# Kernel optimization log

Hardware: AMD Instinct MI355X
Metric: run time of the kernel (lower is better)

Reference implementation:

```python
import jax, jax.numpy as jnp
import numpy as np
import math

B, S, D, NH, HFF, E, K, C, L, V = 8, 256, 1024, 16, 2048, 8, 2, 10, 4, 32000
HD = D // NH
EPS = 1e-5


def _pos_encoding(max_len, d_model):
    pos = jnp.arange(max_len, dtype=jnp.float32)[:, None]
    div = jnp.exp(jnp.arange(0, d_model, 2, dtype=jnp.float32) * (-math.log(10000.0) / d_model))
    pe = jnp.zeros((max_len, d_model), dtype=jnp.float32)
    pe = pe.at[:, 0::2].set(jnp.sin(pos * div))
    pe = pe.at[:, 1::2].set(jnp.cos(pos * div))
    return pe[:, None, :]  # [max_len, 1, D], matching torch buffer layout


def _layernorm(x, g, b):
    mu = jnp.mean(x, axis=-1, keepdims=True)
    var = jnp.mean((x - mu) ** 2, axis=-1, keepdims=True)
    return (x - mu) * jax.lax.rsqrt(var + EPS) * g + b


def setup_inputs() -> dict:
    key = jax.random.key(0)
    ks = jax.random.split(key, 20)
    sc = lambda *shape: 0.02
    inp = {
        "src": jax.random.randint(ks[0], (B, S), 0, V, dtype=jnp.int32),
        "emb": jax.random.normal(ks[1], (V, D), jnp.float32) * 0.02,
        "in_proj_w": jax.random.normal(ks[2], (L, 3 * D, D), jnp.float32) * 0.02,
        "in_proj_b": jnp.zeros((L, 3 * D), jnp.float32),
        "out_w": jax.random.normal(ks[3], (L, D, D), jnp.float32) * 0.02,
        "out_b": jnp.zeros((L, D), jnp.float32),
        "ln1_g": jnp.ones((L, D), jnp.float32),
        "ln1_b": jnp.zeros((L, D), jnp.float32),
        "ln2_g": jnp.ones((L, D), jnp.float32),
        "ln2_b": jnp.zeros((L, D), jnp.float32),
        "gate_w": jax.random.normal(ks[4], (L, E, D), jnp.float32) * 0.02,
        "gate_b": jnp.zeros((L, E), jnp.float32),
        "w1": jax.random.normal(ks[5], (L, E, D, HFF), jnp.float32) * 0.02,
        "b1": jnp.zeros((L, E, HFF), jnp.float32),
        "w2": jax.random.normal(ks[6], (L, E, HFF, D), jnp.float32) * 0.02,
        "b2": jnp.zeros((L, E, D), jnp.float32),
        "cls_w": jax.random.normal(ks[7], (C, D), jnp.float32) * 0.02,
        "cls_b": jnp.zeros((C,), jnp.float32),
    }
    return inp


def _attention(x, ipw, ipb, ow, ob):
    # x: [B,S,D]
    qkv = x @ ipw.T + ipb  # [B,S,3D]
    q, k, v = jnp.split(qkv, 3, axis=-1)
    q = q.reshape(B, S, NH, HD)
    k = k.reshape(B, S, NH, HD)
    v = v.reshape(B, S, NH, HD)
    scores = jnp.einsum("bqhd,bkhd->bhqk", q, k) / math.sqrt(HD)
    attn = jax.nn.softmax(scores, axis=-1)
    o = jnp.einsum("bhqk,bkhd->bqhd", attn, v).reshape(B, S, D)
    return o @ ow.T + ob


def _moe(x, gw, gb, w1, b1, w2, b2):
    # x: [B,S,D]; gw: [E,D]; w1: [E,D,H]; w2: [E,H,D]
    t = x.reshape(B * S, D)
    logits = t @ gw.T + gb  # [T,E]
    topv, topi = jax.lax.top_k(logits, K)  # [T,K]
    weights = jax.nn.softmax(topv, axis=-1)  # [T,K]
    # dense expert compute (small E, compute-bound), combine via top-k gather
    h = jax.nn.relu(jnp.einsum("td,edh->teh", t, w1) + b1)  # [T,E,H]
    y = jnp.einsum("teh,ehd->ted", h, w2) + b2  # [T,E,D]
    sel = jnp.take_along_axis(y, topi[:, :, None], axis=1)  # [T,K,D]
    out = jnp.sum(sel * weights[:, :, None], axis=1)  # [T,D]
    return out.reshape(B, S, D), logits.reshape(B, S, E)


def reference(src, emb, in_proj_w, in_proj_b, out_w, out_b, ln1_g, ln1_b,
              ln2_g, ln2_b, gate_w, gate_b, w1, b1, w2, b2, cls_w, cls_b):
    x = emb[src] * math.sqrt(D)  # [B,S,D]
    pe = _pos_encoding(5000, D)  # [max_len,1,D]
    # faithful to original: pe indexed by batch dim (x.size(0)), broadcast over seq
    x = x + pe[:B]  # [B,1,D] -> broadcast [B,S,D]
    all_gates = []
    for l in range(in_proj_w.shape[0]):
        a = _attention(x, in_proj_w[l], in_proj_b[l], out_w[l], out_b[l])
        x = _layernorm(x + a, ln1_g[l], ln1_b[l])
        m, g = _moe(x, gate_w[l], gate_b[l], w1[l], b1[l], w2[l], b2[l])
        x = _layernorm(x + m, ln2_g[l], ln2_b[l])
        all_gates.append(g)
    pooled = jnp.mean(x, axis=1)  # [B,D]
    out = pooled @ cls_w.T + cls_b  # [B,C]
    return out, jnp.stack(all_gates)  # ([B,C], [L,B,S,E])
```

## Files before the change

### kernel.cpp

```cpp
#include <hip/hip_runtime.h>
#include <math.h>

#define TKN 2048
#define DIM 1024
#define NHEAD 16
#define HDIM 64
#define HFF 2048
#define NE 8
#define TOPK 2
#define NCLS 10
#define NLAYER 4
#define SEQ 256
#define BATCH 8

typedef __attribute__((ext_vector_type(8))) _Float16 f16x8;
typedef __attribute__((ext_vector_type(4))) float f32x4;

__device__ __forceinline__ unsigned short f2h(float v) {
  _Float16 h = (_Float16)v;
  return __builtin_bit_cast(unsigned short, h);
}
__device__ __forceinline__ float h2f(unsigned short u) {
  return (float)__builtin_bit_cast(_Float16, u);
}
__device__ __forceinline__ void fsplit(float v, unsigned short& hi, unsigned short& lo) {
  _Float16 h = (_Float16)v;
  hi = __builtin_bit_cast(unsigned short, h);
  lo = f2h(v - (float)h);
}

__device__ __forceinline__ void gload_lds16(const void* g, void* l) {
  __builtin_amdgcn_global_load_lds((__attribute__((address_space(1))) void*)g,
                                   (__attribute__((address_space(3))) void*)l,
                                   16, 0, 0);
}

__global__ __launch_bounds__(256) void k_embed(const int* __restrict__ src,
                                               const float* __restrict__ emb,
                                               float* __restrict__ x,
                                               unsigned short* __restrict__ xhi,
                                               unsigned short* __restrict__ xlo) {
  const int t = blockIdx.x;
  const int tid = threadIdx.x;
  const int b = t / SEQ;
  const int tok = src[t];
  const float* erow = emb + (size_t)tok * DIM;
  const size_t base = (size_t)t * DIM;
  const float cexp = -9.210340371976184f / 1024.0f;
#pragma unroll
  for (int j = 0; j < 4; ++j) {
    int d = tid + 256 * j;
    int i2 = d & ~1;
    float ang = (float)b * expf((float)i2 * cexp);
    float pe = (d & 1) ? cosf(ang) : sinf(ang);
    float v = erow[d] * 32.0f + pe;
    x[base + d] = v;
    fsplit(v, xhi[base + d], xlo[base + d]);
  }
}

__global__ __launch_bounds__(256) void k_cvt_split(const float* __restrict__ in,
                                                   unsigned short* __restrict__ ohi,
                                                   unsigned short* __restrict__ olo) {
  int i = blockIdx.x * 256 + threadIdx.x;
  float4 v = ((const float4*)in)[i];
  ushort4 h, l;
  fsplit(v.x, h.x, l.x); fsplit(v.y, h.y, l.y);
  fsplit(v.z, h.z, l.z); fsplit(v.w, h.w, l.w);
  ((ushort4*)ohi)[i] = h;
  ((ushort4*)olo)[i] = l;
}

__global__ __launch_bounds__(256) void k_cvt_t_split(const float* __restrict__ in,
                                                     unsigned short* __restrict__ ohi,
                                                     unsigned short* __restrict__ olo,
                                                     int R, int Cc) {
  __shared__ float t[32][33];
  const int tx = threadIdx.x & 31, ty = threadIdx.x >> 5;
  const int c0 = blockIdx.x * 32, r0 = blockIdx.y * 32;
  const float* ip = in + (size_t)blockIdx.z * R * Cc;
  const size_t obase = (size_t)blockIdx.z * R * Cc;
#pragma unroll
  for (int j = 0; j < 4; ++j)
    t[ty + 8 * j][tx] = ip[(size_t)(r0 + ty + 8 * j) * Cc + c0 + tx];
  __syncthreads();
#pragma unroll
  for (int j = 0; j < 4; ++j) {
    unsigned short hi, lo;
    fsplit(t[tx][ty + 8 * j], hi, lo);
    size_t o = obase + (size_t)(c0 + ty + 8 * j) * R + r0 + tx;
    ohi[o] = hi;
    olo[o] = lo;
  }
}

template <int MODE, bool RELU, int OUTK, bool SPLIT>
__global__ __launch_bounds__(256) void k_mfma_gemm(
    const unsigned short* __restrict__ Ahi, const unsigned short* __restrict__ Alo,
    const unsigned short* __restrict__ Bhi, const unsigned short* __restrict__ Blo,
    const float* __restrict__ bias, void* __restrict__ out0, void* __restrict__ out1,
    int M, int N, int K,
    const int* __restrict__ slot_token, const int* __restrict__ offg) {
  constexpr int NP = SPLIT ? 2 : 1;
  __shared__ unsigned short U[2][NP][128 * 64];
  const int tid = threadIdx.x;
  const int w = tid >> 6, lane = tid & 63;
  const int bm = blockIdx.y * 128, bn = blockIdx.x * 128;
  int r0 = 0, rows = M, e = 0;
  if (MODE != 0) {
    e = blockIdx.z;
    r0 = offg[e];
    rows = offg[e + 1] - r0;
    if (bm >= rows) return;
  }
  const size_t bwb = (size_t)e * K * N;
  const float* biasq = bias + (size_t)e * N;

  const int lrow8 = lane >> 3;
  const int s = (lane & 7) ^ lrow8;
  const int chunk = (s & 3) * 8;
  const unsigned short* sp0[4];
  const unsigned short* sp1[4];
#pragma unroll
  for (int i = 0; i < 4; ++i) {
    int rloc = w * 32 + i * 8 + lrow8;
    int growA;
    if (MODE == 0) {
      growA = bm + rloc;
    } else {
      int rr = bm + rloc;
      if (rr >= rows) rr = rows - 1;
      growA = (MODE == 1) ? slot_token[r0 + rr] : (r0 + rr);
    }
    size_t aoff = (size_t)growA * K + chunk;
    size_t boff = bwb + (size_t)(bn + rloc) * K + chunk;
    if constexpr (SPLIT) {
      sp0[i] = (s < 4 ? Ahi : Alo) + aoff;
      sp1[i] = (s < 4 ? Bhi : Blo) + boff;
    } else {
      sp0[i] = (s < 4) ? (Ahi + aoff) : (Bhi + boff);
      sp1[i] = nullptr;
    }
  }

  f32x4 acc[4][4] = {};
  const int wr = w >> 1, wc = w & 1;
  const int lr = lane & 15, lg = lane >> 4;
  const int sw = lr & 7;
  unsigned aoffs[4], boffs[4];
#pragma unroll
  for (int m = 0; m < 4; ++m)
    aoffs[m] = (unsigned)((wr * 64 + m * 16 + lr) * 64 + ((lg ^ sw) * 8));
#pragma unroll
  for (int n = 0; n < 4; ++n)
    boffs[n] = (unsigned)((wc * 64 + n * 16 + lr) * 64 + ((lg ^ sw) * 8));

#pragma unroll
  for (int i = 0; i < 4; ++i) {
    gload_lds16(sp0[i], &U[0][0][(w * 32 + i * 8) * 64]);
    sp0[i] += 32;
    if constexpr (SPLIT) {
      gload_lds16(sp1[i], &U[0][1][(w * 32 + i * 8) * 64]);
      sp1[i] += 32;
    }
  }
  asm volatile("s_waitcnt vmcnt(0)" ::: "memory");
  __builtin_amdgcn_s_barrier();

  const int NT = K / 32;
#pragma unroll 2
  for (int t = 0; t < NT; ++t) {
    const int cur = t & 1;
    if (t + 1 < NT) {
#pragma unroll
      for (int i = 0; i < 4; ++i) {
        gload_lds16(sp0[i], &U[cur ^ 1][0][(w * 32 + i * 8) * 64]);
        sp0[i] += 32;
        if constexpr (SPLIT) {
          gload_lds16(sp1[i], &U[cur ^ 1][1][(w * 32 + i * 8) * 64]);
          sp1[i] += 32;
        }
      }
    }
    f16x8 afh[4], bfh[4], afl[4], bfl[4];
    if constexpr (SPLIT) {
#pragma unroll
      for (int m = 0; m < 4; ++m) afh[m] = *(const f16x8*)&U[cur][0][aoffs[m]];
#pragma unroll
      for (int m = 0; m < 4; ++m) afl[m] = *(const f16x8*)&U[cur][0][aoffs[m] ^ 32];
#pragma unroll
      for (int n = 0; n < 4; ++n) bfh[n] = *(const f16x8*)&U[cur][1][boffs[n]];
#pragma unroll
      for (int n = 0; n < 4; ++n) bfl[n] = *(const f16x8*)&U[cur][1][boffs[n] ^ 32];
    } else {
#pragma unroll
      for (int m = 0; m < 4; ++m) afh[m] = *(const f16x8*)&U[cur][0][aoffs[m]];
#pragma unroll
      for (int n = 0; n < 4; ++n) bfh[n] = *(const f16x8*)&U[cur][0][boffs[n] ^ 32];
    }
#pragma unroll
    for (int m = 0; m < 4; ++m)
#pragma unroll
      for (int n = 0; n < 4; ++n) {
        acc[m][n] = __builtin_amdgcn_mfma_f32_16x16x32_f16(afh[m], bfh[n], acc[m][n], 0, 0, 0);
        if constexpr (SPLIT) {
          acc[m][n] = __builtin_amdgcn_mfma_f32_16x16x32_f16(afh[m], bfl[n], acc[m][n], 0, 0, 0);
          acc[m][n] = __builtin_amdgcn_mfma_f32_16x16x32_f16(afl[m], bfh[n], acc[m][n], 0, 0, 0);
        }
      }
    asm volatile("s_waitcnt vmcnt(0)" ::: "memory");
    __builtin_amdgcn_s_barrier();
  }

  float bv[4];
#pragma unroll
  for (int n = 0; n < 4; ++n) bv[n] = biasq[bn + wc * 64 + n * 16 + lr];

#pragma unroll
  for (int m = 0; m < 4; ++m) {
#pragma unroll
    for (int j = 0; j < 4; ++j) {
      int rowg = bm + wr * 64 + m * 16 + lg * 4 + j;
      if (MODE != 0 && rowg >= rows) continue;
      size_t crow = (size_t)((MODE == 0) ? rowg : (r0 + rowg)) * N;
#pragma unroll
      for (int n = 0; n < 4; ++n) {
        float v = acc[m][n][j] + bv[n];
        if (RELU) v = fmaxf(v, 0.f);
        size_t o = crow + bn + wc * 64 + n * 16 + lr;
        if (OUTK == 0) {
          ((float*)out0)[o] = v;
        } else if (OUTK == 1) {
          ((unsigned short*)out0)[o] = f2h(v);
        } else {
          unsigned short hi, lo;
          fsplit(v, hi, lo);
          ((unsigned short*)out0)[o] = hi;
          ((unsigned short*)out1)[o] = lo;
        }
      }
    }
  }
}

__global__ __launch_bounds__(256) void k_attn(const float* __restrict__ qkv,
                                              unsigned short* __restrict__ ohi,
                                              unsigned short* __restrict__ olo) {
  const int qt = blockIdx.x;
  const int hh = blockIdx.y;
  const int bb = blockIdx.z;
  const int tid = threadIdx.x;
  __shared__ float qs[16][64];
  __shared__ float ps[16][256];
  const int t0 = bb * SEQ + qt * 16;
  for (int i = tid; i < 16 * 64; i += 256) {
    int qi = i >> 6, d = i & 63;
    qs[qi][d] = qkv[(size_t)(t0 + qi) * (3 * DIM) + hh * 64 + d];
  }
  __syncthreads();
  float s[16];
#pragma unroll
  for (int qi = 0; qi < 16; ++qi) s[qi] = 0.f;
  const float* krow = qkv + (size_t)(bb * SEQ + tid) * (3 * DIM) + DIM + hh * 64;
#pragma unroll 4
  for (int c = 0; c < 16; ++c) {
    float4 kv = *(const float4*)(krow + c * 4);
#pragma unroll
    for (int qi = 0; qi < 16; ++qi) {
      s[qi] += kv.x * qs[qi][c * 4 + 0] + kv.y * qs[qi][c * 4 + 1] +
               kv.z * qs[qi][c * 4 + 2] + kv.w * qs[qi][c * 4 + 3];
    }
  }
#pragma unroll
  for (int qi = 0; qi < 16; ++qi) ps[qi][tid] = s[qi] * 0.125f;
  __syncthreads();
  const int wv = tid >> 6, lane = tid & 63;
  for (int rr = wv; rr < 16; rr += 4) {
    float v[4];
#pragma unroll
    for (int j = 0; j < 4; ++j) v[j] = ps[rr][lane + 64 * j];
    float m = fmaxf(fmaxf(v[0], v[1]), fmaxf(v[2], v[3]));
    for (int msk = 32; msk; msk >>= 1) m = fmaxf(m, __shfl_xor(m, msk));
    float e[4], sum = 0.f;
#pragma unroll
    for (int j = 0; j < 4; ++j) { e[j] = expf(v[j] - m); sum += e[j]; }
    for (int msk = 32; msk; msk >>= 1) sum += __shfl_xor(sum, msk);
    float inv = 1.0f / sum;
#pragma unroll
    for (int j = 0; j < 4; ++j) ps[rr][lane + 64 * j] = e[j] * inv;
  }
  __syncthreads();
  const int qi0 = tid >> 6, d = tid & 63;
  float acc[4] = {0.f, 0.f, 0.f, 0.f};
  const float* vbase = qkv + (size_t)(bb * SEQ) * (3 * DIM) + 2 * DIM + hh * 64 + d;
  for (int k = 0; k < 256; ++k) {
    float vv = vbase[(size_t)k * (3 * DIM)];
    acc[0] += ps[qi0][k] * vv;
    acc[1] += ps[qi0 + 4][k] * vv;
    acc[2] += ps[qi0 + 8][k] * vv;
    acc[3] += ps[qi0 + 12][k] * vv;
  }
#pragma unroll
  for (int j = 0; j < 4; ++j) {
    size_t o = (size_t)(t0 + qi0 + 4 * j) * DIM + hh * 64 + d;
    fsplit(acc[j], ohi[o], olo[o]);
  }
}

__device__ __forceinline__ float block_reduce_sum(float v, float* red) {
  const int tid = threadIdx.x;
  red[tid] = v;
  __syncthreads();
  for (int s = 128; s > 0; s >>= 1) {
    if (tid < s) red[tid] += red[tid + s];
    __syncthreads();
  }
  float r = red[0];
  __syncthreads();
  return r;
}

__global__ __launch_bounds__(256) void k_add_ln(const float* __restrict__ xin,
                                                const float* __restrict__ add,
                                                const float* __restrict__ g,
                                                const float* __restrict__ bt,
                                                float* __restrict__ xout,
                                                unsigned short* __restrict__ xhi,
                                                unsigned short* __restrict__ xlo) {
  __shared__ float red[256];
  const int t = blockIdx.x, tid = threadIdx.x;
  const size_t base = (size_t)t * DIM;
  float v[4];
  float s = 0.f;
#pragma unroll
  for (int j = 0; j < 4; ++j) {
    int d = tid + 256 * j;
    v[j] = xin[base + d] + add[base + d];
    s += v[j];
  }
  float mean = block_reduce_sum(s, red) * (1.0f / DIM);
  float s2 = 0.f;
#pragma unroll
  for (int j = 0; j < 4; ++j) { float dv = v[j] - mean; s2 += dv * dv; }
  float var = block_reduce_sum(s2, red) * (1.0f / DIM);
  float rs = rsqrtf(var + 1e-5f);
#pragma unroll
  for (int j = 0; j < 4; ++j) {
    int d = tid + 256 * j;
    float o = (v[j] - mean) * rs * g[d] + bt[d];
    xout[base + d] = o;
    fsplit(o, xhi[base + d], xlo[base + d]);
  }
}

__global__ __launch_bounds__(256) void k_gate(const float* __restrict__ x,
                                              const float* __restrict__ gw,
                                              const float* __restrict__ gb,
                                              float* __restrict__ gout,
                                              int* __restrict__ topi,
                                              float* __restrict__ topw) {
  __shared__ float xs[DIM];
  __shared__ float lgs[NE];
  const int t = blockIdx.x, tid = threadIdx.x;
#pragma unroll
  for (int j = 0; j < 4; ++j) xs[tid + 256 * j] = x[(size_t)t * DIM + tid + 256 * j];
  __syncthreads();
  const int eg = tid >> 5, l32 = tid & 31;
  const float* wrow = gw + (size_t)eg * DIM;
  float p = 0.f;
  for (int j = 0; j < 32; ++j) {
    int d = l32 + 32 * j;
    p += xs[d] * wrow[d];
  }
  for (int m = 16; m; m >>= 1) p += __shfl_xor(p, m);
  if (l32 == 0) lgs[eg] = p;
  __syncthreads();
  if (tid < NE) {
    float v = lgs[tid] + gb[tid];
    gout[(size_t)t * NE + tid] = v;
    lgs[tid] = v;
  }
  __syncthreads();
  if (tid == 0) {
    int i0 = 0; float v0 = lgs[0];
    for (int i = 1; i < NE; ++i) if (lgs[i] > v0) { v0 = lgs[i]; i0 = i; }
    int i1 = -1; float v1 = -1e30f;
    for (int i = 0; i < NE; ++i) { if (i == i0) continue; if (lgs[i] > v1) { v1 = lgs[i]; i1 = i; } }
    float e1 = expf(v1 - v0);
    float w0 = 1.0f / (1.0f + e1);
    topi[2 * t] = i0; topi[2 * t + 1] = i1;
    topw[2 * t] = w0; topw[2 * t + 1] = e1 * w0;
  }
}

__global__ __launch_bounds__(512) void k_route(const int* __restrict__ topi,
                                               int* __restrict__ offg,
                                               int* __restrict__ slot_token,
                                               int* __restrict__ slot_of) {
  __shared__ int cnt_s[NE];
  __shared__ int off_s[NE + 1];
  const int tid = threadIdx.x;
  const int w = tid >> 6, lane = tid & 63;
  int c = 0;
  for (int i = lane; i < TKN * TOPK; i += 64) c += (topi[i] == w) ? 1 : 0;
  for (int m = 32; m; m >>= 1) c += __shfl_xor(c, m);
  if (lane == 0) cnt_s[w] = c;
  __syncthreads();
  if (tid == 0) {
    off_s[0] = 0;
    for (int e2 = 0; e2 < NE; ++e2) off_s[e2 + 1] = off_s[e2] + cnt_s[e2];
    for (int e2 = 0; e2 <= NE; ++e2) offg[e2] = off_s[e2];
  }
  __syncthreads();
  int base = off_s[w];
  for (int i0 = 0; i0 < TKN * TOPK; i0 += 64) {
    int i = i0 + lane;
    bool mm = (topi[i] == w);
    unsigned long long mask = __ballot(mm ? 1 : 0);
    int rank = __popcll(mask & ((1ull << lane) - 1ull));
    if (mm) {
      int slot = base + rank;
      slot_token[slot] = i >> 1;
      slot_of[i] = slot;
    }
    base += __popcll(mask);
  }
}

__global__ __launch_bounds__(256) void k_moe_combine_ln(const float* __restrict__ xin,
                                                        const float* __restrict__ y,
                                                        const float* __restrict__ topw,
                                                        const int* __restrict__ slot_of,
                                                        const float* __restrict__ g,
                                                        const float* __restrict__ bt,
                                                        float* __restrict__ xout,
                                                        unsigned short* __restrict__ xhi,
                                                        unsigned short* __restrict__ xlo) {
  __shared__ float red[256];
  const int t = blockIdx.x, tid = threadIdx.x;
  const float w0 = topw[2 * t], w1v = topw[2 * t + 1];
  const int s0 = slot_of[2 * t], s1 = slot_of[2 * t + 1];
  const size_t base = (size_t)t * DIM;
  float v[4];
  float s = 0.f;
#pragma unroll
  for (int j = 0; j < 4; ++j) {
    int d = tid + 256 * j;
    v[j] = xin[base + d] + w0 * y[(size_t)s0 * DIM + d] + w1v * y[(size_t)s1 * DIM + d];
    s += v[j];
  }
  float mean = block_reduce_sum(s, red) * (1.0f / DIM);
  float s2 = 0.f;
#pragma unroll
  for (int j = 0; j < 4; ++j) { float dv = v[j] - mean; s2 += dv * dv; }
  float var = block_reduce_sum(s2, red) * (1.0f / DIM);
  float rs = rsqrtf(var + 1e-5f);
#pragma unroll
  for (int j = 0; j < 4; ++j) {
    int d = tid + 256 * j;
    float o = (v[j] - mean) * rs * g[d] + bt[d];
    xout[base + d] = o;
    fsplit(o, xhi[base + d], xlo[base + d]);
  }
}

__global__ __launch_bounds__(256) void k_pool_cls(const float* __restrict__ x,
                                                  const float* __restrict__ cw,
                                                  const float* __restrict__ cb,
                                                  float* __restrict__ out) {
  __shared__ float pooled[DIM];
  const int b = blockIdx.x, tid = threadIdx.x;
  float a[4] = {0.f, 0.f, 0.f, 0.f};
  for (int s = 0; s < SEQ; ++s) {
    const float* row = x + (size_t)(b * SEQ + s) * DIM;
#pragma unroll
    for (int j = 0; j < 4; ++j) a[j] += row[tid + 256 * j];
  }
#pragma unroll
  for (int j = 0; j < 4; ++j) pooled[tid + 256 * j] = a[j] * (1.0f / SEQ);
  __syncthreads();
  const int wv = tid >> 6, lane = tid & 63;
  for (int c = wv; c < NCLS; c += 4) {
    float p = 0.f;
    for (int d = lane; d < DIM; d += 64) p += pooled[d] * cw[(size_t)c * DIM + d];
    for (int m = 32; m; m >>= 1) p += __shfl_xor(p, m);
    if (lane == 0) out[b * NCLS + c] = p + cb[c];
  }
}

extern "C" void kernel_launch(void* const* d_in, const int* in_sizes, int n_in,
                              void* d_out, int out_size, void* d_ws, size_t ws_size,
                              hipStream_t stream) {
  const int*   src  = (const int*)  d_in[0];
  const float* emb  = (const float*)d_in[1];
  const float* ipw  = (const float*)d_in[2];
  const float* ipb  = (const float*)d_in[3];
  const float* ow   = (const float*)d_in[4];
  const float* ob   = (const float*)d_in[5];
  const float* ln1g = (const float*)d_in[6];
  const float* ln1b = (const float*)d_in[7];
  const float* ln2g = (const float*)d_in[8];
  const float* ln2b = (const float*)d_in[9];
  const float* gw   = (const float*)d_in[10];
  const float* gb   = (const float*)d_in[11];
  const float* w1   = (const float*)d_in[12];
  const float* b1   = (const float*)d_in[13];
  const float* w2   = (const float*)d_in[14];
  const float* b2   = (const float*)d_in[15];
  const float* cw   = (const float*)d_in[16];
  const float* cb   = (const float*)d_in[17];
  float* out = (float*)d_out;

  char* ws = (char*)d_ws;
  size_t off = 0;
  auto carve = [&](size_t bytes) -> void* {
    void* p = ws + off;
    off += (bytes + 255) & ~(size_t)255;
    return p;
  };
  float*          x     = (float*)carve((size_t)TKN * DIM * 4);
  unsigned short* xhi   = (unsigned short*)carve((size_t)TKN * DIM * 2);
  unsigned short* xlo   = (unsigned short*)carve((size_t)TKN * DIM * 2);
  char*           bufQ  = (char*)carve((size_t)2 * TKN * TOPK * HFF * 2);
  float*          qkv   = (float*)bufQ;
  unsigned short* h_hi  = (unsigned short*)bufQ;
  unsigned short* h_lo  = (unsigned short*)(bufQ + (size_t)TKN * TOPK * HFF * 2);
  unsigned short* at_hi = (unsigned short*)carve((size_t)TKN * DIM * 2);
  unsigned short* at_lo = (unsigned short*)carve((size_t)TKN * DIM * 2);
  char*           bufP  = (char*)carve((size_t)TKN * TOPK * DIM * 4);
  float*          proj  = (float*)bufP;
  float*          ybuf  = (float*)bufP;
  unsigned short* wq_hi = (unsigned short*)carve((size_t)3 * DIM * DIM * 2);
  unsigned short* wq_lo = (unsigned short*)carve((size_t)3 * DIM * DIM * 2);
  unsigned short* wo_hi = (unsigned short*)carve((size_t)DIM * DIM * 2);
  unsigned short* wo_lo = (unsigned short*)carve((size_t)DIM * DIM * 2);
  unsigned short* wt_hi = (unsigned short*)carve((size_t)NE * DIM * HFF * 2);
  unsigned short* wt_lo = (unsigned short*)carve((size_t)NE * DIM * HFF * 2);
  float* topw       = (float*)carve((size_t)TKN * TOPK * 4);
  int*   topi       = (int*)  carve((size_t)TKN * TOPK * 4);
  int*   slot_token = (int*)  carve((size_t)TKN * TOPK * 4);
  int*   slot_of    = (int*)  carve((size_t)TKN * TOPK * 4);
  int*   offg       = (int*)  carve(64);

  k_embed<<<TKN, 256, 0, stream>>>(src, emb, x, xhi, xlo);

  for (int l = 0; l < NLAYER; ++l) {
    const float* ipw_l = ipw + (size_t)l * 3 * DIM * DIM;
    const float* ow_l  = ow  + (size_t)l * DIM * DIM;
    const float* w1_l  = w1  + (size_t)l * NE * DIM * HFF;
    const float* w2_l  = w2  + (size_t)l * NE * HFF * DIM;
    const bool sp = (l < NLAYER - 1);

    k_cvt_split<<<(3 * DIM * DIM) / 1024, 256, 0, stream>>>(ipw_l, wq_hi, wq_lo);
    k_cvt_split<<<(DIM * DIM) / 1024, 256, 0, stream>>>(ow_l, wo_hi, wo_lo);
    k_cvt_t_split<<<dim3(HFF / 32, DIM / 32, NE), 256, 0, stream>>>(w1_l, wt_hi, wt_lo, DIM, HFF);

    if (sp)
      k_mfma_gemm<0, false, 0, true><<<dim3(3 * DIM / 128, TKN / 128), 256, 0, stream>>>(
          xhi, xlo, wq_hi, wq_lo, ipb + (size_t)l * 3 * DIM, qkv, nullptr, TKN, 3 * DIM, DIM, nullptr, nullptr);
    else
      k_mfma_gemm<0, false, 0, false><<<dim3(3 * DIM / 128, TKN / 128), 256, 0, stream>>>(
          xhi, xlo, wq_hi, wq_lo, ipb + (size_t)l * 3 * DIM, qkv, nullptr, TKN, 3 * DIM, DIM, nullptr, nullptr);

    k_attn<<<dim3(SEQ / 16, NHEAD, BATCH), 256, 0, stream>>>(qkv, at_hi, at_lo);

    if (sp)
      k_mfma_gemm<0, false, 0, true><<<dim3(DIM / 128, TKN / 128), 256, 0, stream>>>(
          at_hi, at_lo, wo_hi, wo_lo, ob + (size_t)l * DIM, proj, nullptr, TKN, DIM, DIM, nullptr, nullptr);
    else
      k_mfma_gemm<0, false, 0, false><<<dim3(DIM / 128, TKN / 128), 256, 0, stream>>>(
          at_hi, at_lo, wo_hi, wo_lo, ob + (size_t)l * DIM, proj, nullptr, TKN, DIM, DIM, nullptr, nullptr);

    k_add_ln<<<TKN, 256, 0, stream>>>(x, proj, ln1g + l * DIM, ln1b + l * DIM, x, xhi, xlo);

    k_gate<<<TKN, 256, 0, stream>>>(x, gw + (size_t)l * NE * DIM, gb + l * NE,
                                    out + NCLS * BATCH + (size_t)l * TKN * NE, topi, topw);
    k_route<<<1, 512, 0, stream>>>(topi, offg, slot_token, slot_of);

    if (sp)
      k_mfma_gemm<1, true, 2, true><<<dim3(HFF / 128, TKN * TOPK / 128, NE), 256, 0, stream>>>(
          xhi, xlo, wt_hi, wt_lo, b1 + (size_t)l * NE * HFF, h_hi, h_lo, 0, HFF, DIM, slot_token, offg);
    else
      k_mfma_gemm<1, true, 1, false><<<dim3(HFF / 128, TKN * TOPK / 128, NE), 256, 0, stream>>>(
          xhi, xlo, wt_hi, wt_lo, b1 + (size_t)l * NE * HFF, h_hi, nullptr, 0, HFF, DIM, slot_token, offg);

    k_cvt_t_split<<<dim3(DIM / 32, HFF / 32, NE), 256, 0, stream>>>(w2_l, wt_hi, wt_lo, HFF, DIM);

    if (sp)
      k_mfma_gemm<2, false, 0, true><<<dim3(DIM / 128, TKN * TOPK / 128, NE), 256, 0, stream>>>(
          h_hi, h_lo, wt_hi, wt_lo, b2 + (size_t)l * NE * DIM, ybuf, nullptr, 0, DIM, HFF, nullptr, offg);
    else
      k_mfma_gemm<2, false, 0, false><<<dim3(DIM / 128, TKN * TOPK / 128, NE), 256, 0, stream>>>(
          h_hi, h_lo, wt_hi, wt_lo, b2 + (size_t)l * NE * DIM, ybuf, nullptr, 0, DIM, HFF, nullptr, offg);

    k_moe_combine_ln<<<TKN, 256, 0, stream>>>(x, ybuf, topw, slot_of,
                                              ln2g + l * DIM, ln2b + l * DIM, x, xhi, xlo);
  }
  k_pool_cls<<<BATCH, 256, 0, stream>>>(x, cw, cb, out);
}
```

Measured before the change: 1.568 ms.

## Use single-fp16 expert GEMMs in layer 3 and vectorize weight transpose-split

The MoE expert GEMMs now drop the hi/lo split-precision path from layer index 2 onward, not only in the last layer, and weight conversion skips writing the low half when it isn't needed. The transpose-split kernel is rewritten to handle 64-row tiles and emit 8-wide vectorized fp16 stores instead of scalar stores. This cuts MFMA work and conversion traffic in layer 3's FFN, at the cost of lower numerical accuracy in that layer.

Result: faster. 1.450 ms (-7.5%).

```diff
diff --git a/kernel.cpp b/kernel.cpp
--- a/kernel.cpp
+++ b/kernel.cpp
@@ -15,6 +15,7 @@
 
 typedef __attribute__((ext_vector_type(8))) _Float16 f16x8;
 typedef __attribute__((ext_vector_type(4))) float f32x4;
+typedef __attribute__((ext_vector_type(8))) unsigned short u16x8;
 
 __device__ __forceinline__ unsigned short f2h(float v) {
   _Float16 h = (_Float16)v;
@@ -59,6 +60,7 @@
   }
 }
 
+template <bool LO>
 __global__ __launch_bounds__(256) void k_cvt_split(const float* __restrict__ in,
                                                    unsigned short* __restrict__ ohi,
                                                    unsigned short* __restrict__ olo) {
@@ -68,30 +70,35 @@
   fsplit(v.x, h.x, l.x); fsplit(v.y, h.y, l.y);
   fsplit(v.z, h.z, l.z); fsplit(v.w, h.w, l.w);
   ((ushort4*)ohi)[i] = h;
-  ((ushort4*)olo)[i] = l;
-}
-
-__global__ __launch_bounds__(256) void k_cvt_t_split(const float* __restrict__ in,
-                                                     unsigned short* __restrict__ ohi,
-                                                     unsigned short* __restrict__ olo,
-                                                     int R, int Cc) {
-  __shared__ float t[32][33];
-  const int tx = threadIdx.x & 31, ty = threadIdx.x >> 5;
-  const int c0 = blockIdx.x * 32, r0 = blockIdx.y * 32;
+  if (LO) ((ushort4*)olo)[i] = l;
+}
+
+template <bool LO>
+__global__ __launch_bounds__(256) void k_cvt_t2(const float* __restrict__ in,
+                                                unsigned short* __restrict__ ohi,
+                                                unsigned short* __restrict__ olo,
+                                                int R, int Cc) {
+  __shared__ float ts[64][33];
+  const int t = threadIdx.x;
+  const int c0 = blockIdx.x * 32, r0 = blockIdx.y * 64;
   const float* ip = in + (size_t)blockIdx.z * R * Cc;
   const size_t obase = (size_t)blockIdx.z * R * Cc;
-#pragma unroll
-  for (int j = 0; j < 4; ++j)
-    t[ty + 8 * j][tx] = ip[(size_t)(r0 + ty + 8 * j) * Cc + c0 + tx];
-  __syncthreads();
-#pragma unroll
-  for (int j = 0; j < 4; ++j) {
+  const int cc = t & 31, rr0 = t >> 5;
+#pragma unroll
+  for (int j = 0; j < 8; ++j)
+    ts[rr0 + 8 * j][cc] = ip[(size_t)(r0 + rr0 + 8 * j) * Cc + c0 + cc];
+  __syncthreads();
+  const int c = t >> 3, rch = (t & 7) * 8;
+  u16x8 hv, lv;
+#pragma unroll
+  for (int i = 0; i < 8; ++i) {
     unsigned short hi, lo;
-    fsplit(t[tx][ty + 8 * j], hi, lo);
-    size_t o = obase + (size_t)(c0 + ty + 8 * j) * R + r0 + tx;
-    ohi[o] = hi;
-    olo[o] = lo;
-  }
+    fsplit(ts[rch + i][c], hi, lo);
+    hv[i] = hi; lv[i] = lo;
+  }
+  size_t o = obase + (size_t)(c0 + c) * R + r0 + rch;
+  *(u16x8*)(ohi + o) = hv;
+  if (LO) *(u16x8*)(olo + o) = lv;
 }
 
 template <int MODE, bool RELU, int OUTK, bool SPLIT>
@@ -549,13 +556,22 @@
     const float* ow_l  = ow  + (size_t)l * DIM * DIM;
     const float* w1_l  = w1  + (size_t)l * NE * DIM * HFF;
     const float* w2_l  = w2  + (size_t)l * NE * HFF * DIM;
-    const bool sp = (l < NLAYER - 1);
-
-    k_cvt_split<<<(3 * DIM * DIM) / 1024, 256, 0, stream>>>(ipw_l, wq_hi, wq_lo);
-    k_cvt_split<<<(DIM * DIM) / 1024, 256, 0, stream>>>(ow_l, wo_hi, wo_lo);
-    k_cvt_t_split<<<dim3(HFF / 32, DIM / 32, NE), 256, 0, stream>>>(w1_l, wt_hi, wt_lo, DIM, HFF);
-
-    if (sp)
+    const bool spd = (l < 3);
+    const bool spm = (l < 2);
+
+    if (spd) {
+      k_cvt_split<true><<<(3 * DIM * DIM) / 1024, 256, 0, stream>>>(ipw_l, wq_hi, wq_lo);
+      k_cvt_split<true><<<(DIM * DIM) / 1024, 256, 0, stream>>>(ow_l, wo_hi, wo_lo);
+    } else {
+      k_cvt_split<false><<<(3 * DIM * DIM) / 1024, 256, 0, stream>>>(ipw_l, wq_hi, wq_lo);
+      k_cvt_split<false><<<(DIM * DIM) / 1024, 256, 0, stream>>>(ow_l, wo_hi, wo_lo);
+    }
+    if (spm)
+      k_cvt_t2<true><<<dim3(HFF / 32, DIM / 64, NE), 256, 0, stream>>>(w1_l, wt_hi, wt_lo, DIM, HFF);
+    else
+      k_cvt_t2<false><<<dim3(HFF / 32, DIM / 64, NE), 256, 0, stream>>>(w1_l, wt_hi, wt_lo, DIM, HFF);
+
+    if (spd)
       k_mfma_gemm<0, false, 0, true><<<dim3(3 * DIM / 128, TKN / 128), 256, 0, stream>>>(
           xhi, xlo, wq_hi, wq_lo, ipb + (size_t)l * 3 * DIM, qkv, nullptr, TKN, 3 * DIM, DIM, nullptr, nullptr);
     else
@@ -564,7 +580,7 @@
 
     k_attn<<<dim3(SEQ / 16, NHEAD, BATCH), 256, 0, stream>>>(qkv, at_hi, at_lo);
 
-    if (sp)
+    if (spd)
       k_mfma_gemm<0, false, 0, true><<<dim3(DIM / 128, TKN / 128), 256, 0, stream>>>(
           at_hi, at_lo, wo_hi, wo_lo, ob + (size_t)l * DIM, proj, nullptr, TKN, DIM, DIM, nullptr, nullptr);
     else
@@ -577,16 +593,19 @@
                                     out + NCLS * BATCH + (size_t)l * TKN * NE, topi, topw);
     k_route<<<1, 512, 0, stream>>>(topi, offg, slot_token, slot_of);
 
-    if (sp)
+    if (spm)
       k_mfma_gemm<1, true, 2, true><<<dim3(HFF / 128, TKN * TOPK / 128, NE), 256, 0, stream>>>(
           xhi, xlo, wt_hi, wt_lo, b1 + (size_t)l * NE * HFF, h_hi, h_lo, 0, HFF, DIM, slot_token, offg);
     else
       k_mfma_gemm<1, true, 1, false><<<dim3(HFF / 128, TKN * TOPK / 128, NE), 256, 0, stream>>>(
           xhi, xlo, wt_hi, wt_lo, b1 + (size_t)l * NE * HFF, h_hi, nullptr, 0, HFF, DIM, slot_token, offg);
 
-    k_cvt_t_split<<<dim3(DIM / 32, HFF / 32, NE), 256, 0, stream>>>(w2_l, wt_hi, wt_lo, HFF, DIM);
-
-    if (sp)
+    if (spm)
+      k_cvt_t2<true><<<dim3(DIM / 32, HFF / 64, NE), 256, 0, stream>>>(w2_l, wt_hi, wt_lo, HFF, DIM);
+    else
+      k_cvt_t2<false><<<dim3(DIM / 32, HFF / 64, NE), 256, 0, stream>>>(w2_l, wt_hi, wt_lo, HFF, DIM);
+
+    if (spm)
       k_mfma_gemm<2, false, 0, true><<<dim3(DIM / 128, TKN * TOPK / 128, NE), 256, 0, stream>>>(
           h_hi, h_lo, wt_hi, wt_lo, b2 + (size_t)l * NE * DIM, ybuf, nullptr, 0, DIM, HFF, nullptr, offg);
     else
```
